# Kernel optimization log

Hardware: AMD Instinct MI355X
Metric: run time of the kernel (lower is better)

Reference implementation:

```python
import itertools
import jax, jax.numpy as jnp
import numpy as np


def setup_inputs() -> dict:
    key = jax.random.key(0)
    k1, k2 = jax.random.split(key)
    B, X, Y, Z, C = 2, 160, 192, 160, 1
    vol = jax.random.normal(k1, (B, X, Y, Z, C), dtype=jnp.float32)
    trf = jax.random.normal(k2, (B, X, Y, Z, 3), dtype=jnp.float32)  # dense displacement field
    return {"vol": vol, "trf": trf}


def _warp(vol, trf):
    # vol: [B, *spatial, C]; trf: [B, *spatial, nd] displacement (indexing='ij')
    B = vol.shape[0]
    spatial = vol.shape[1:-1]
    nd = len(spatial)
    C = vol.shape[-1]
    N = int(np.prod(spatial))

    grids = jnp.meshgrid(*[jnp.arange(s, dtype=jnp.float32) for s in spatial], indexing="ij")
    # absolute sample locations per dim: [B, *spatial]
    loc = [grids[d][None] + trf[..., d] for d in range(nd)]

    max_loc = [s - 1 for s in spatial]
    loc0 = [jnp.clip(jnp.floor(loc[d]), 0.0, max_loc[d]) for d in range(nd)]
    loc1 = [jnp.clip(loc0[d] + 1.0, 0.0, max_loc[d]) for d in range(nd)]
    clipped = [jnp.clip(loc[d], 0.0, max_loc[d]) for d in range(nd)]
    # neurite weight convention: weight for corner bit 0 is (loc1 - loc), for bit 1 is (1 - that)
    w1 = [loc1[d] - clipped[d] for d in range(nd)]   # weight when corner uses loc0
    w0 = [1.0 - w1[d] for d in range(nd)]            # weight when corner uses loc1
    i0 = [loc0[d].astype(jnp.int32) for d in range(nd)]
    i1 = [loc1[d].astype(jnp.int32) for d in range(nd)]

    vol_flat = vol.reshape(B, N, C)

    out = jnp.zeros((B,) + spatial + (C,), dtype=vol.dtype)
    for corner in itertools.product([0, 1], repeat=nd):
        subs = [(i1[d] if corner[d] else i0[d]) for d in range(nd)]
        ind = subs[0]
        for d in range(1, nd):
            ind = ind * spatial[d] + subs[d]  # row-major sub2ind
        vals = jnp.take_along_axis(vol_flat, ind.reshape(B, N)[..., None], axis=1)
        vals = vals.reshape((B,) + spatial + (C,))
        wt = (w0[0] if corner[0] else w1[0])
        for d in range(1, nd):
            wt = wt * (w0[d] if corner[d] else w1[d])
        out = out + wt[..., None] * vals
    return out


def reference(vol, trf):
    # indexing='ij', single_transform=False, fill_value=None (clamp to edge), linear interp.
    # The layer also passes trf through unchanged; we return the warped volume.
    return _warp(vol, trf)
```

## Files before the change

### kernel.cpp

```cpp
#include <hip/hip_runtime.h>

constexpr int B = 2, X = 160, Y = 192, Z = 160;
constexpr int TXs = 8, TYs = 8, TZs = 16;
constexpr int XT = X / TXs, YT = Y / TYs, ZT = Z / TZs;
constexpr int NTILES = B * XT * YT * ZT;
constexpr int NXCD = 8;
constexpr int CHUNK = NTILES / NXCD;
constexpr int RX = 15, RY = 16, RZ = 24;
constexpr int RSTRIDE = 27;
constexpr int NROWS = RX * RY;
constexpr int LDSF = NROWS * RSTRIDE;
constexpr int NCHUNKS = NROWS * 6;

typedef float f32x4 __attribute__((ext_vector_type(4)));
typedef float f32x2a __attribute__((ext_vector_type(2), aligned(4)));

__global__ __launch_bounds__(256, 6) void warp_kernel(
    const float* __restrict__ vol,
    const float* __restrict__ trf,
    float* __restrict__ out)
{
    __shared__ float lds[LDSF];

    const int tid = threadIdx.x;
    const int bid = blockIdx.x;

    const int eff = (bid & (NXCD - 1)) * CHUNK + (bid >> 3);

    int tz = eff % ZT;
    int r  = eff / ZT;
    int ty = r % YT;
    int r2 = r / YT;
    int tx = r2 % XT;
    int b  = r2 / XT;

    const int xs = tx * TXs - 4;
    const int ys = ty * TYs - 4;
    const int zs = tz * TZs - 4;
    const int bX = b * X;

    {
#pragma unroll
        for (int k = 0; k < 6; ++k) {
            unsigned c = (unsigned)tid + k * 256u;
            if (c < (unsigned)NCHUNKS) {
                unsigned row = c / 6u;
                unsigned j   = c - 6u * row;
                int xi  = (int)(row >> 4);
                int yi  = (int)(row & 15u);
                int xg  = min(max(xs + xi, 0), X - 1);
                int yg  = min(max(ys + yi, 0), Y - 1);
                int zg  = min(max(zs + 4 * (int)j, 0), Z - 4);
                const f32x4 v = *reinterpret_cast<const f32x4*>(
                    vol + ((size_t)(bX + xg) * Y + yg) * Z + zg);
                int a = (int)row * RSTRIDE + 4 * (int)j;
                lds[a + 0] = v.x;
                lds[a + 1] = v.y;
                lds[a + 2] = v.z;
                lds[a + 3] = v.w;
            }
        }
    }
    __syncthreads();

    int zq = tid & 3;
    int ly = (tid >> 2) & 7;
    int lx = tid >> 5;
    int x  = tx * TXs + lx;
    int y  = ty * TYs + ly;
    int z0v = tz * TZs + 4 * zq;

    size_t vid0 = ((size_t)(bX + x) * Y + y) * Z + z0v;

    const f32x4* tp = reinterpret_cast<const f32x4*>(trf + vid0 * 3);
    f32x4 t0 = tp[0], t1 = tp[1], t2 = tp[2];
    float d[12] = {t0.x, t0.y, t0.z, t0.w,
                   t1.x, t1.y, t1.z, t1.w,
                   t2.x, t2.y, t2.z, t2.w};

    const float mx = (float)(X - 1), my = (float)(Y - 1), mz = (float)(Z - 1);
    const float fxc = (float)x, fyc = (float)y;

    float res[4];
#pragma unroll
    for (int e = 0; e < 4; ++e) {
        float lxf = fxc + d[3 * e + 0];
        float lyf = fyc + d[3 * e + 1];
        float lzf = (float)(z0v + e) + d[3 * e + 2];

        float clx = fminf(fmaxf(lxf, 0.0f), mx);
        float flx = floorf(clx);
        float fx  = clx - flx;
        int   ix0 = (int)flx;

        float cly = fminf(fmaxf(lyf, 0.0f), my);
        float fly = floorf(cly);
        float fy  = cly - fly;
        int   iy0 = (int)fly;

        float clz = fminf(fmaxf(lzf, 0.0f), mz);
        float flz = floorf(clz);
        float fz  = clz - flz;
        int   iz0 = (int)flz;

        int ux0 = ix0 - xs, uy0 = iy0 - ys, uz0 = iz0 - zs;

        bool ok = ((unsigned)ux0 < (unsigned)(RX - 1)) &
                  ((unsigned)uy0 < (unsigned)(RY - 1)) &
                  ((unsigned)uz0 < (unsigned)(RZ - 1));

        float v000, v001, v010, v011, v100, v101, v110, v111;
        if (ok) {
            int w = ((ux0 << 4) + uy0) * RSTRIDE + uz0;
            f32x2a p00 = *reinterpret_cast<const f32x2a*>(&lds[w]);
            f32x2a p01 = *reinterpret_cast<const f32x2a*>(&lds[w + RSTRIDE]);
            f32x2a p10 = *reinterpret_cast<const f32x2a*>(&lds[w + 16 * RSTRIDE]);
            f32x2a p11 = *reinterpret_cast<const f32x2a*>(&lds[w + 17 * RSTRIDE]);
            v000 = p00.x; v001 = p00.y;
            v010 = p01.x; v011 = p01.y;
            v100 = p10.x; v101 = p10.y;
            v110 = p11.x; v111 = p11.y;
        } else {
            int ix1 = min(ix0 + 1, X - 1);
            int iy1 = min(iy0 + 1, Y - 1);
            int iz1 = min(iz0 + 1, Z - 1);
            size_t g00 = ((size_t)(bX + ix0) * Y + iy0) * Z;
            size_t g01 = ((size_t)(bX + ix0) * Y + iy1) * Z;
            size_t g10 = ((size_t)(bX + ix1) * Y + iy0) * Z;
            size_t g11 = ((size_t)(bX + ix1) * Y + iy1) * Z;
            v000 = vol[g00 + iz0];
            v001 = vol[g00 + iz1];
            v010 = vol[g01 + iz0];
            v011 = vol[g01 + iz1];
            v100 = vol[g10 + iz0];
            v101 = vol[g10 + iz1];
            v110 = vol[g11 + iz0];
            v111 = vol[g11 + iz1];
        }

        float c00 = v000 + fz * (v001 - v000);
        float c01 = v010 + fz * (v011 - v010);
        float c10 = v100 + fz * (v101 - v100);
        float c11 = v110 + fz * (v111 - v110);
        float c0  = c00 + fy * (c01 - c00);
        float c1  = c10 + fy * (c11 - c10);
        res[e] = c0 + fx * (c1 - c0);
    }

    f32x4 o;
    o.x = res[0]; o.y = res[1]; o.z = res[2]; o.w = res[3];
    *reinterpret_cast<f32x4*>(out + vid0) = o;
}

extern "C" void kernel_launch(void* const* d_in, const int* in_sizes, int n_in,
                              void* d_out, int out_size, void* d_ws, size_t ws_size,
                              hipStream_t stream) {
    const float* vol = (const float*)d_in[0];
    const float* trf = (const float*)d_in[1];
    float* out = (float*)d_out;

    warp_kernel<<<NTILES, 256, 0, stream>>>(vol, trf, out);
}
```

Measured before the change: 41.70 us.

## Double threads per tile to 512 with two voxels per thread and cheaper indexing

New measurement: 42.40 us. About the same (+1.7%).

```diff
diff --git a/kernel.cpp b/kernel.cpp
--- a/kernel.cpp
+++ b/kernel.cpp
@@ -15,7 +15,7 @@
 typedef float f32x4 __attribute__((ext_vector_type(4)));
 typedef float f32x2a __attribute__((ext_vector_type(2), aligned(4)));
 
-__global__ __launch_bounds__(256, 6) void warp_kernel(
+__global__ __launch_bounds__(512, 8) void warp_kernel(
     const float* __restrict__ vol,
     const float* __restrict__ trf,
     float* __restrict__ out)
@@ -40,70 +40,64 @@
     const int bX = b * X;
 
     {
+        int row = (tid * 171) >> 10;
+        int j   = tid - 6 * row;
 #pragma unroll
-        for (int k = 0; k < 6; ++k) {
-            unsigned c = (unsigned)tid + k * 256u;
-            if (c < (unsigned)NCHUNKS) {
-                unsigned row = c / 6u;
-                unsigned j   = c - 6u * row;
-                int xi  = (int)(row >> 4);
-                int yi  = (int)(row & 15u);
-                int xg  = min(max(xs + xi, 0), X - 1);
-                int yg  = min(max(ys + yi, 0), Y - 1);
-                int zg  = min(max(zs + 4 * (int)j, 0), Z - 4);
+        for (int k = 0; k < 3; ++k) {
+            if (k < 2 || tid < NCHUNKS - 1024) {
+                int xi = row >> 4;
+                int yi = row & 15;
+                int xg = min(max(xs + xi, 0), X - 1);
+                int yg = min(max(ys + yi, 0), Y - 1);
+                int zg = min(max(zs + 4 * j, 0), Z - 4);
                 const f32x4 v = *reinterpret_cast<const f32x4*>(
                     vol + ((size_t)(bX + xg) * Y + yg) * Z + zg);
-                int a = (int)row * RSTRIDE + 4 * (int)j;
+                int a = row * RSTRIDE + 4 * j;
                 lds[a + 0] = v.x;
                 lds[a + 1] = v.y;
                 lds[a + 2] = v.z;
                 lds[a + 3] = v.w;
             }
+            int jn = j + 2;
+            bool wrap = (jn >= 6);
+            j   = wrap ? jn - 6 : jn;
+            row += wrap ? 86 : 85;
         }
     }
     __syncthreads();
 
-    int zq = tid & 3;
-    int ly = (tid >> 2) & 7;
-    int lx = tid >> 5;
+    int zq = tid & 7;
+    int ly = (tid >> 3) & 7;
+    int lx = tid >> 6;
     int x  = tx * TXs + lx;
     int y  = ty * TYs + ly;
-    int z0v = tz * TZs + 4 * zq;
+    int z0v = tz * TZs + 2 * zq;
 
     size_t vid0 = ((size_t)(bX + x) * Y + y) * Z + z0v;
 
-    const f32x4* tp = reinterpret_cast<const f32x4*>(trf + vid0 * 3);
-    f32x4 t0 = tp[0], t1 = tp[1], t2 = tp[2];
-    float d[12] = {t0.x, t0.y, t0.z, t0.w,
-                   t1.x, t1.y, t1.z, t1.w,
-                   t2.x, t2.y, t2.z, t2.w};
+    const float* tb = trf + vid0 * 3;
+    f32x4 ta = *reinterpret_cast<const f32x4*>(tb);
+    f32x2a tc = *reinterpret_cast<const f32x2a*>(tb + 4);
+    float d[6] = {ta.x, ta.y, ta.z, ta.w, tc.x, tc.y};
 
     const float mx = (float)(X - 1), my = (float)(Y - 1), mz = (float)(Z - 1);
     const float fxc = (float)x, fyc = (float)y;
+    const float xsf = (float)xs, ysf = (float)ys, zsf = (float)zs;
 
-    float res[4];
+    float res[2];
 #pragma unroll
-    for (int e = 0; e < 4; ++e) {
+    for (int e = 0; e < 2; ++e) {
         float lxf = fxc + d[3 * e + 0];
         float lyf = fyc + d[3 * e + 1];
         float lzf = (float)(z0v + e) + d[3 * e + 2];
 
-        float clx = fminf(fmaxf(lxf, 0.0f), mx);
-        float flx = floorf(clx);
-        float fx  = clx - flx;
-        int   ix0 = (int)flx;
+        float rxf = __builtin_amdgcn_fmed3f(lxf, 0.0f, mx) - xsf;
+        float ryf = __builtin_amdgcn_fmed3f(lyf, 0.0f, my) - ysf;
+        float rzf = __builtin_amdgcn_fmed3f(lzf, 0.0f, mz) - zsf;
 
-        float cly = fminf(fmaxf(lyf, 0.0f), my);
-        float fly = floorf(cly);
-        float fy  = cly - fly;
-        int   iy0 = (int)fly;
-
-        float clz = fminf(fmaxf(lzf, 0.0f), mz);
-        float flz = floorf(clz);
-        float fz  = clz - flz;
-        int   iz0 = (int)flz;
-
-        int ux0 = ix0 - xs, uy0 = iy0 - ys, uz0 = iz0 - zs;
+        float flx = floorf(rxf), fly = floorf(ryf), flz = floorf(rzf);
+        int ux0 = (int)flx, uy0 = (int)fly, uz0 = (int)flz;
+        float fx = rxf - flx, fy = ryf - fly, fz = rzf - flz;
 
         bool ok = ((unsigned)ux0 < (unsigned)(RX - 1)) &
                   ((unsigned)uy0 < (unsigned)(RY - 1)) &
@@ -121,6 +115,10 @@
             v100 = p10.x; v101 = p10.y;
             v110 = p11.x; v111 = p11.y;
         } else {
+            int ix0 = ux0 + xs, iy0 = uy0 + ys, iz0 = uz0 + zs;
+            ix0 = min(max(ix0, 0), X - 1);
+            iy0 = min(max(iy0, 0), Y - 1);
+            iz0 = min(max(iz0, 0), Z - 1);
             int ix1 = min(ix0 + 1, X - 1);
             int iy1 = min(iy0 + 1, Y - 1);
             int iz1 = min(iz0 + 1, Z - 1);
@@ -147,9 +145,9 @@
         res[e] = c0 + fx * (c1 - c0);
     }
 
-    f32x4 o;
-    o.x = res[0]; o.y = res[1]; o.z = res[2]; o.w = res[3];
-    *reinterpret_cast<f32x4*>(out + vid0) = o;
+    f32x2a o;
+    o.x = res[0]; o.y = res[1];
+    *reinterpret_cast<f32x2a*>(out + vid0) = o;
 }
 
 extern "C" void kernel_launch(void* const* d_in, const int* in_sizes, int n_in,
@@ -159,5 +157,5 @@
     const float* trf = (const float*)d_in[1];
     float* out = (float*)d_out;
 
-    warp_kernel<<<NTILES, 256, 0, stream>>>(vol, trf, out);
+    warp_kernel<<<NTILES, 512, 0, stream>>>(vol, trf, out);
 }
```
